# Optimization experiments

Hardware: AMD Instinct MI355X
Metric: run time of the kernel (lower is better)

Reference implementation:

```python
import jax, jax.numpy as jnp
import numpy as np

DMODEL = 1024
DK = 64
DHEAD = 16
DEPTH = DK * DHEAD
N, LQ, L = 4, 4096, 4096
FAC1 = 1.0 / np.sqrt(DK)  # relu kernel scale folded into omega, as in reset()
EPS = 1e-6


def setup_inputs() -> dict:
    key = jax.random.key(0)
    ks = jax.random.split(key, 10)
    x = jax.random.normal(ks[0], (N, LQ, DMODEL), jnp.float32)
    y = jax.random.normal(ks[1], (N, L, DMODEL), jnp.float32)
    s_in = 1.0 / np.sqrt(DMODEL)
    s_depth = 1.0 / np.sqrt(DEPTH)
    # Linear weights stored as (in, out) so application is x @ W + b
    WQ = jax.random.normal(ks[2], (DMODEL, DEPTH), jnp.float32) * s_in
    WK = jax.random.normal(ks[3], (DMODEL, DEPTH), jnp.float32) * s_in
    WV = jax.random.normal(ks[4], (DMODEL, DEPTH), jnp.float32) * s_in
    WO = jax.random.normal(ks[5], (DEPTH, DMODEL), jnp.float32) * s_depth
    bQ = jnp.zeros((DEPTH,), jnp.float32)
    bK = jnp.zeros((DEPTH,), jnp.float32)
    bV = jnp.zeros((DEPTH,), jnp.float32)
    bO = jnp.zeros((DMODEL,), jnp.float32)
    # orthogonal random-feature projection: QR of gaussian, scaled by sqrt(dk), then *fac1 (relu)
    g = np.random.default_rng(0).standard_normal((DK, DK)).astype(np.float32)
    qmat, _ = np.linalg.qr(g)
    omega = jnp.asarray(qmat * np.sqrt(DK) * FAC1, dtype=jnp.float32)
    return dict(x=x, y=y, WQ=WQ, bQ=bQ, WK=WK, bK=bK, WV=WV, bV=bV,
                WO=WO, bO=bO, omega=omega)


def reference(x, y, WQ, bQ, WK, bK, WV, bV, WO, bO, omega):
    n, lq, _ = x.shape
    l = y.shape[1]
    # project and split heads: (n, h, L, dk)
    q = (x @ WQ + bQ).reshape(n, lq, DHEAD, DK).transpose(0, 2, 1, 3)
    k = (y @ WK + bK).reshape(n, l, DHEAD, DK).transpose(0, 2, 1, 3)
    v = (y @ WV + bV).reshape(n, l, DHEAD, DK).transpose(0, 2, 1, 3)
    # relu random-feature map phi(x) = relu(x @ omega) + eps
    q = jax.nn.relu(q @ omega) + EPS
    k = jax.nn.relu(k @ omega) + EPS
    # linear attention: out = phi(q) @ (phi(k)^T @ v) / (phi(q) @ phi(k)^T @ 1)
    kv = jnp.einsum('nhld,nhle->nhde', k, v)          # (n, h, dk, dk)
    ksum = jnp.sum(k, axis=2)                          # (n, h, dk)
    d_inv = jnp.einsum('nhqd,nhd->nhq', q, ksum)[..., None]
    out = jnp.einsum('nhqd,nhde->nhqe', q, kv) / d_inv  # (n, h, Lq, dk)
    out = out.transpose(0, 2, 1, 3).reshape(n, lq, DEPTH)
    return out @ WO + bO
```

## Files before the change

kernel.cpp:

```cpp
#include <hip/hip_runtime.h>

#define EPSF 1e-6f

typedef _Float16 f16x8 __attribute__((ext_vector_type(8)));
typedef _Float16 f16x4 __attribute__((ext_vector_type(4)));
typedef float    f32x4 __attribute__((ext_vector_type(4)));

#define GLL16(gp, lp) __builtin_amdgcn_global_load_lds( \
    (const __attribute__((address_space(1))) void*)(gp), \
    (__attribute__((address_space(3))) void*)(lp), 16, 0, 0)

__global__ __launch_bounds__(256) void cvt_f16(const float* __restrict__ in,
                                               _Float16* __restrict__ out, int n8) {
    int idx = blockIdx.x * 256 + threadIdx.x;
    int stride = gridDim.x * 256;
    for (; idx < n8; idx += stride) {
        const float4* p = (const float4*)in + (size_t)idx * 2;
        float4 a = p[0], b = p[1];
        f16x8 o;
        o[0] = (_Float16)a.x; o[1] = (_Float16)a.y; o[2] = (_Float16)a.z; o[3] = (_Float16)a.w;
        o[4] = (_Float16)b.x; o[5] = (_Float16)b.y; o[6] = (_Float16)b.z; o[7] = (_Float16)b.w;
        *(f16x8*)(out + (size_t)idx * 8) = o;
    }
}

__global__ __launch_bounds__(256) void build_obdT(const float* __restrict__ omega,
                                                  _Float16* __restrict__ obdT) {
    int idx = blockIdx.x * 256 + threadIdx.x;
    int c = idx >> 10, k = idx & 1023;
    float v = ((c >> 6) == (k >> 6)) ? omega[(k & 63) * 64 + (c & 63)] : 0.f;
    obdT[idx] = (_Float16)v;
}

__global__ __launch_bounds__(256) void transpose_cvt(const float* __restrict__ in,
                                                     _Float16* __restrict__ out) {
    __shared__ float tile[64][65];
    const int t = threadIdx.x;
    const int k0 = blockIdx.x * 64, n0 = blockIdx.y * 64;
#pragma unroll
    for (int j = 0; j < 16; j++) {
        int idx = j * 256 + t; int r = idx >> 6, c = idx & 63;
        tile[r][c] = in[(size_t)(k0 + r) * 1024 + n0 + c];
    }
    __syncthreads();
#pragma unroll
    for (int j = 0; j < 16; j++) {
        int idx = j * 256 + t; int rn = idx >> 6, ck = idx & 63;
        out[(size_t)(n0 + rn) * 1024 + k0 + ck] = (_Float16)tile[ck][rn];
    }
}

__global__ __launch_bounds__(256) void fold_bias(const float* __restrict__ b,
                                                 const float* __restrict__ omega,
                                                 float* __restrict__ bout) {
    int c = blockIdx.x * 256 + threadIdx.x;
    int h = c >> 6, e = c & 63;
    float s = 0.f;
    for (int d = 0; d < 64; d++) s += b[h * 64 + d] * omega[d * 64 + e];
    bout[c] = s;
}

__global__ __launch_bounds__(256) void copy_f32(const float* __restrict__ in,
                                                float* __restrict__ out, int n) {
    int i = blockIdx.x * 256 + threadIdx.x;
    if (i < n) out[i] = in[i];
}

__global__ __launch_bounds__(256) void gemm_fold(const _Float16* __restrict__ A,
                                                 const _Float16* __restrict__ Bt,
                                                 _Float16* __restrict__ out0,
                                                 _Float16* __restrict__ out1) {
    const int K = 1024;
    __shared__ __align__(16) _Float16 Asm[128 * 32];
    __shared__ __align__(16) _Float16 Bsm[128 * 32];
    const int t = threadIdx.x, lane = t & 63, w = t >> 6;
    const int bm = blockIdx.y * 128, bn = blockIdx.x * 128;
    const int wm = (w >> 1) * 64, wn = (w & 1) * 64;
    const int r15 = lane & 15, slog = lane >> 4;

    int aoff[4], boff[4];
#pragma unroll
    for (int m = 0; m < 4; m++) {
        int ra = wm + m * 16 + r15;
        aoff[m] = ra * 32 + (slog ^ ((ra >> 1) & 3)) * 8;
        int rb = wn + m * 16 + r15;
        boff[m] = rb * 32 + (slog ^ ((rb >> 1) & 3)) * 8;
    }
    f32x4 acc[4][4];
#pragma unroll
    for (int m = 0; m < 4; m++)
#pragma unroll
        for (int n = 0; n < 4; n++) acc[m][n] = (f32x4){0.f, 0.f, 0.f, 0.f};

    for (int kt = 0; kt < K; kt += 32) {
        __syncthreads();
#pragma unroll
        for (int i = 0; i < 2; i++) {
            int seg = i * 256 + w * 64 + lane;
            int r = seg >> 2, sp = seg & 3;
            int sg = sp ^ ((r >> 1) & 3);
            GLL16(A  + (size_t)(bm + r) * K + kt + sg * 8, Asm + (size_t)(i * 256 + w * 64) * 8);
            GLL16(Bt + (size_t)(bn + r) * K + kt + sg * 8, Bsm + (size_t)(i * 256 + w * 64) * 8);
        }
        __syncthreads();
        f16x8 av[4], bv[4];
#pragma unroll
        for (int m = 0; m < 4; m++) av[m] = *(const f16x8*)(Asm + aoff[m]);
#pragma unroll
        for (int n = 0; n < 4; n++) bv[n] = *(const f16x8*)(Bsm + boff[n]);
#pragma unroll
        for (int m = 0; m < 4; m++)
#pragma unroll
            for (int n = 0; n < 4; n++)
                acc[m][n] = __builtin_amdgcn_mfma_f32_16x16x32_f16(av[m], bv[n], acc[m][n], 0, 0, 0);
    }

#pragma unroll
    for (int m = 0; m < 4; m++) {
        int row0 = bm + wm + m * 16 + slog * 4;
        _Float16* C = (row0 < 1024) ? out0 : out1;
        int l = row0 & 1023;
#pragma unroll
        for (int n = 0; n < 4; n++) {
            int colg = bn + wn + n * 16 + r15;
            f16x4 p;
#pragma unroll
            for (int j = 0; j < 4; j++) p[j] = (_Float16)acc[m][n][j];
            *(f16x4*)(C + (size_t)colg * 1024 + l) = p;
        }
    }
}

template<int EPI>
__global__ __launch_bounds__(512, 2) void gemm256(const _Float16* __restrict__ A,
                                                  const _Float16* __restrict__ Bt,
                                                  const float* __restrict__ bias,
                                                  void* __restrict__ out0,
                                                  void* __restrict__ out1,
                                                  int M, int N, int K, int nbn) {
    __shared__ __align__(16) char lds[131072];
    const int t = threadIdx.x, lane = t & 63, w = t >> 6;
    const int nwg = gridDim.x;
    const int f = (blockIdx.x & 7) * (nwg >> 3) + (blockIdx.x >> 3);
    const int bm = (f / nbn) * 256, bn = (f % nbn) * 256;
    const int wm = (w & 1) * 128, wn = (w >> 1) * 64;
    const int r15 = lane & 15, hi = lane >> 4;
    const int srow = lane >> 2, sp = lane & 3;

    int aoff[8], boff[4];
#pragma unroll
    for (int m = 0; m < 8; m++) {
        int r = wm + m * 16 + r15;
        aoff[m] = r * 64 + (((hi + (r >> 1)) & 3) << 4);
    }
#pragma unroll
    for (int n = 0; n < 4; n++) {
        int r = wn + n * 16 + r15;
        boff[n] = r * 64 + (((hi + (r >> 1)) & 3) << 4);
    }

    f32x4 acc[8][4];
#pragma unroll
    for (int m = 0; m < 8; m++)
#pragma unroll
        for (int n = 0; n < 4; n++) acc[m][n] = (f32x4){0.f, 0.f, 0.f, 0.f};

    auto stage = [&](int s) {
        char* base = lds + (s & 3) * 32768;
        int kt = s * 32;
#pragma unroll
        for (int p = 0; p < 2; p++) {
            int row = w * 32 + p * 16 + srow;
            int sg = (sp - ((row >> 1) & 3)) & 3;
            GLL16(A  + (size_t)(bm + row) * K + kt + sg * 8, base + w * 2048 + p * 1024);
            GLL16(Bt + (size_t)(bn + row) * K + kt + sg * 8, base + 16384 + w * 2048 + p * 1024);
        }
    };

    const int NS = K >> 5;
    stage(0); stage(1); stage(2);
    for (int s = 0; s < NS; ++s) {
        if (s + 2 < NS)      asm volatile("s_waitcnt vmcnt(8)" ::: "memory");
        else if (s + 1 < NS) asm volatile("s_waitcnt vmcnt(4)" ::: "memory");
        else                 asm volatile("s_waitcnt vmcnt(0)" ::: "memory");
        asm volatile("s_barrier" ::: "memory");
        if (s + 3 < NS) stage(s + 3);
        const char* La = lds + (s & 3) * 32768;
        const char* Lb = La + 16384;
        f16x8 bv[4];
#pragma unroll
        for (int n = 0; n < 4; n++) bv[n] = *(const f16x8*)(Lb + boff[n]);
        f16x8 av[8];
#pragma unroll
        for (int m = 0; m < 8; m++) av[m] = *(const f16x8*)(La + aoff[m]);
        __builtin_amdgcn_s_setprio(1);
#pragma unroll
        for (int m = 0; m < 8; m++)
#pragma unroll
            for (int n = 0; n < 4; n++)
                acc[m][n] = __builtin_amdgcn_mfma_f32_16x16x32_f16(av[m], bv[n], acc[m][n], 0, 0, 0);
        __builtin_amdgcn_s_setprio(0);
    }

    if (EPI == 3) {
        asm volatile("s_barrier" ::: "memory");
        char* LW = lds + w * 16384;
        const int colg0 = bn + wn;
        const bool isK = colg0 < 1024;
        _Float16* Cb = isK ? (_Float16*)out0 : (_Float16*)out1;
        const int hd = (isK ? colg0 : colg0 - 1024) >> 6;
        const int nb = bm >> 12;
        const int l0 = (bm & 4095) + wm;
#pragma unroll
        for (int m = 0; m < 8; m++)
#pragma unroll
            for (int n = 0; n < 4; n++) {
                int d = n * 16 + r15;
                float bs = bias[colg0 + d];
                f16x4 pk;
#pragma unroll
                for (int j = 0; j < 4; j++) {
                    float xv = acc[m][n][j] + bs;
                    if (isK) xv = fmaxf(xv, 0.f) + EPSF;
                    pk[j] = (_Float16)xv;
                }
                *(f16x4*)(LW + d * 256 + ((m * 32 + hi * 8) ^ ((d & 15) << 4))) = pk;
            }
        _Float16* basep = Cb + (size_t)(nb * 16 + hd) * 64 * 4096 + l0;
#pragma unroll
        for (int pass = 0; pass < 16; pass++) {
            int d = pass * 4 + hi;
            f16x8 v = *(const f16x8*)(LW + d * 256 + ((r15 * 16) ^ ((d & 15) << 4)));
            *(f16x8*)(basep + (size_t)d * 4096 + r15 * 8) = v;
        }
    } else {
#pragma unroll
        for (int m = 0; m < 8; m++) {
            int row0 = bm + wm + m * 16 + hi * 4;
#pragma unroll
            for (int n = 0; n < 4; n++) {
                int colg = bn + wn + n * 16 + r15;
                float bs = bias ? bias[colg] : 0.f;
#pragma unroll
                for (int j = 0; j < 4; j++) {
                    float xv = acc[m][n][j] + bs;
                    if (EPI == 1) {
                        xv = fmaxf(xv, 0.f) + EPSF;
                        ((_Float16*)out0)[(size_t)(row0 + j) * N + colg] = (_Float16)xv;
                    } else {
                        ((float*)out0)[(size_t)(row0 + j) * N + colg] = xv;
                    }
                }
            }
        }
    }
}

__global__ __launch_bounds__(256) void ksum_kernel(const _Float16* __restrict__ KphiT,
                                                   float* __restrict__ ksum) {
    const int t = threadIdx.x, lane = t & 63, w = t >> 6;
    const int gid = blockIdx.x;
    const int head = gid >> 4;
    const int d = (gid & 15) * 4 + w;
    const _Float16* src = KphiT + ((size_t)head * 64 + d) * 4096;
    float s = 0.f;
#pragma unroll
    for (int i = 0; i < 8; i++) {
        f16x8 v = *(const f16x8*)(src + (size_t)(i * 64 + lane) * 8);
#pragma unroll
        for (int j = 0; j < 8; j++) s += (float)v[j];
    }
#pragma unroll
    for (int o = 32; o; o >>= 1) s += __shfl_xor(s, o, 64);
    if (lane == 0) ksum[(size_t)head * 64 + d] = s;
}

__global__ __launch_bounds__(256) void kvt_kernel(const _Float16* __restrict__ Vt,
                                                  const _Float16* __restrict__ KphiT,
                                                  float* __restrict__ kvpart) {
    const int t = threadIdx.x, lane = t & 63, w = t >> 6;
    const int head = blockIdx.y;
    const int l0 = blockIdx.x * 1024;
    __shared__ __align__(16) _Float16 As[64 * 128];
    __shared__ __align__(16) _Float16 Bs[64 * 128];
    const int r15 = lane & 15, slog = lane >> 4;
    f32x4 acc[4][4];
#pragma unroll
    for (int m = 0; m < 4; m++)
#pragma unroll
        for (int n = 0; n < 4; n++) acc[m][n] = (f32x4){0.f, 0.f, 0.f, 0.f};

    for (int it = 0; it < 8; it++) {
        __syncthreads();
        int lbase = l0 + it * 128;
#pragma unroll
        for (int i = 0; i < 4; i++) {
            int seg = i * 256 + w * 64 + lane;
            int r = seg >> 4, sp2 = seg & 15;
            int sg = sp2 ^ (r & 15);
            GLL16(Vt    + ((size_t)head * 64 + r) * 4096 + lbase + sg * 8, As + (size_t)(i * 256 + w * 64) * 8);
            GLL16(KphiT + ((size_t)head * 64 + r) * 4096 + lbase + sg * 8, Bs + (size_t)(i * 256 + w * 64) * 8);
        }
        __syncthreads();
        f16x8 av[4], bv[4];
#pragma unroll
        for (int m = 0; m < 4; m++) {
            int r = m * 16 + r15;
            int s2 = w * 4 + slog;
            int ph = s2 ^ (r & 15);
            av[m] = *(const f16x8*)(As + r * 128 + ph * 8);
            bv[m] = *(const f16x8*)(Bs + r * 128 + ph * 8);
        }
#pragma unroll
        for (int m = 0; m < 4; m++)
#pragma unroll
            for (int n = 0; n < 4; n++)
                acc[m][n] = __builtin_amdgcn_mfma_f32_16x16x32_f16(av[m], bv[n], acc[m][n], 0, 0, 0);
    }
    float* red = (float*)As;
    for (int ww = 0; ww < 4; ww++) {
        __syncthreads();
        if (w == ww) {
#pragma unroll
            for (int m = 0; m < 4; m++)
#pragma unroll
                for (int n = 0; n < 4; n++)
#pragma unroll
                    for (int j = 0; j < 4; j++) {
                        int row = m * 16 + slog * 4 + j, col = n * 16 + r15;
                        if (ww == 0) red[row * 64 + col] = acc[m][n][j];
                        else         red[row * 64 + col] += acc[m][n][j];
                    }
        }
    }
    __syncthreads();
    float* outp = kvpart + ((size_t)head * 4 + blockIdx.x) * 4096;
#pragma unroll
    for (int i = 0; i < 16; i++) { int idx = i * 256 + t; outp[idx] = red[idx]; }
}

__global__ __launch_bounds__(256) void kvreduce(const float* __restrict__ kvpart,
                                                float* __restrict__ kvT) {
    int head = blockIdx.x, t = threadIdx.x;
#pragma unroll
    for (int i = 0; i < 16; i++) {
        int idx = i * 256 + t;
        float s = 0.f;
#pragma unroll
        for (int c = 0; c < 4; c++) s += kvpart[((size_t)head * 4 + c) * 4096 + idx];
        kvT[(size_t)head * 4096 + idx] = s;
    }
}

__global__ __launch_bounds__(256) void numdiv_kernel(const _Float16* __restrict__ Qphi,
                                                     const float* __restrict__ kvT,
                                                     const float* __restrict__ ksum,
                                                     _Float16* __restrict__ U) {
    const int t = threadIdx.x, lane = t & 63, w = t >> 6;
    const int h = blockIdx.y;
    const int m0 = blockIdx.x * 256;
    const int nb = m0 >> 12;
    const int head = nb * 16 + h;
    __shared__ __align__(16) _Float16 Qs[256 * 64];
    __shared__ __align__(16) _Float16 Bs[64 * 64];
    __shared__ float ksl[64];

#pragma unroll
    for (int i = 0; i < 8; i++) {
        int seg = i * 256 + w * 64 + lane;
        int r = seg >> 3, sp = seg & 7;
        int sg = sp ^ (r & 7);
        GLL16(Qphi + (size_t)(m0 + r) * 1024 + h * 64 + sg * 8, Qs + (size_t)(i * 256 + w * 64) * 8);
    }
#pragma unroll
    for (int i = 0; i < 2; i++) {
        int sidx = i * 256 + t;
        int r = sidx >> 3, p = sidx & 7;
        int sg = p ^ (r & 7);
        const float4* src = (const float4*)(kvT + (size_t)head * 4096 + r * 64 + sg * 8);
        float4 v0 = src[0], v1 = src[1];
        f16x8 o;
        o[0] = (_Float16)v0.x; o[1] = (_Float16)v0.y; o[2] = (_Float16)v0.z; o[3] = (_Float16)v0.w;
        o[4] = (_Float16)v1.x; o[5] = (_Float16)v1.y; o[6] = (_Float16)v1.z; o[7] = (_Float16)v1.w;
        *(f16x8*)(Bs + sidx * 8) = o;
    }
    if (t < 64) ksl[t] = ksum[(size_t)head * 64 + t];
    __syncthreads();

    const int r15 = lane & 15, slog = lane >> 4;
    f32x4 acc[4][4];
#pragma unroll
    for (int m = 0; m < 4; m++)
#pragma unroll
        for (int n = 0; n < 4; n++) acc[m][n] = (f32x4){0.f, 0.f, 0.f, 0.f};
    float dp[4] = {0.f, 0.f, 0.f, 0.f};

#pragma unroll
    for (int kk = 0; kk < 2; kk++) {
        float ks[8];
#pragma unroll
        for (int j = 0; j < 8; j++) ks[j] = ksl[kk * 32 + slog * 8 + j];
        f16x8 av[4], bv[4];
#pragma unroll
        for (int m = 0; m < 4; m++) {
            int r = w * 64 + m * 16 + r15;
            int ph = (kk * 4 + slog) ^ (r & 7);
            av[m] = *(const f16x8*)(Qs + r * 64 + ph * 8);
        }
#pragma unroll
        for (int n = 0; n < 4; n++) {
            int r = n * 16 + r15;
            int ph = (kk * 4 + slog) ^ (r & 7);
            bv[n] = *(const f16x8*)(Bs + r * 64 + ph * 8);
        }
#pragma unroll
        for (int m = 0; m < 4; m++)
#pragma unroll
            for (int j = 0; j < 8; j++) dp[m] += (float)av[m][j] * ks[j];
#pragma unroll
        for (int m = 0; m < 4; m++)
#pragma unroll
            for (int n = 0; n < 4; n++)
                acc[m][n] = __builtin_amdgcn_mfma_f32_16x16x32_f16(av[m], bv[n], acc[m][n], 0, 0, 0);
    }
#pragma unroll
    for (int m = 0; m < 4; m++) {
        dp[m] += __shfl_xor(dp[m], 16, 64);
        dp[m] += __shfl_xor(dp[m], 32, 64);
    }
#pragma unroll
    for (int m = 0; m < 4; m++) {
#pragma unroll
        for (int j = 0; j < 4; j++) {
            float den = __shfl(dp[m], slog * 4 + j, 64);
            float inv = __builtin_amdgcn_rcpf(den);
            int row = m0 + w * 64 + m * 16 + slog * 4 + j;
#pragma unroll
            for (int n = 0; n < 4; n++)
                U[(size_t)row * 1024 + h * 64 + n * 16 + r15] = (_Float16)(acc[m][n][j] * inv);
        }
    }
}

extern "C" void kernel_launch(void* const* d_in, const int* in_sizes, int n_in,
                              void* d_out, int out_size, void* d_ws, size_t ws_size,
                              hipStream_t stream) {
    (void)in_sizes; (void)n_in; (void)out_size; (void)ws_size;
    const float* x     = (const float*)d_in[0];
    const float* y     = (const float*)d_in[1];
    const float* WQ    = (const float*)d_in[2];
    const float* bQ    = (const float*)d_in[3];
    const float* WK    = (const float*)d_in[4];
    const float* bK    = (const float*)d_in[5];
    const float* WV    = (const float*)d_in[6];
    const float* bV    = (const float*)d_in[7];
    const float* WO    = (const float*)d_in[8];
    const float* bO    = (const float*)d_in[9];
    const float* omega = (const float*)d_in[10];

    char* ws = (char*)d_ws;
    size_t off = 0;
    auto alloc = [&](size_t bytes) { void* p = ws + off; off += (bytes + 255) & ~(size_t)255; return p; };
    const size_t BIG = (size_t)16384 * 1024 * 2;
    _Float16* xb    = (_Float16*)alloc(BIG);
    _Float16* yb    = (_Float16*)alloc(BIG);
    _Float16* WQKb  = (_Float16*)alloc((size_t)2048 * 1024 * 2);
    _Float16* obdT  = (_Float16*)alloc(1024 * 1024 * 2);
    _Float16* Wqt   = (_Float16*)alloc(1024 * 1024 * 2);
    _Float16* Wkvt  = (_Float16*)alloc((size_t)2048 * 1024 * 2);
    _Float16* Wot   = (_Float16*)alloc(1024 * 1024 * 2);
    float*    bQf   = (float*)alloc(1024 * 4);
    float*    bkv   = (float*)alloc(2048 * 4);
    _Float16* Qphi  = (_Float16*)alloc(BIG);
    _Float16* KphiT = (_Float16*)alloc(BIG);
    _Float16* Vt    = (_Float16*)alloc(BIG);
    float*    kvpart= (float*)alloc((size_t)256 * 4096 * 4);
    float*    kvT   = (float*)alloc((size_t)64 * 4096 * 4);
    float*    ksum  = (float*)alloc((size_t)64 * 64 * 4);
    _Float16* U     = xb;

    cvt_f16<<<2048, 256, 0, stream>>>(x, xb, 16384 * 1024 / 8);
    cvt_f16<<<2048, 256, 0, stream>>>(y, yb, 16384 * 1024 / 8);
    cvt_f16<<<512, 256, 0, stream>>>(WQ, WQKb, 1024 * 1024 / 8);
    cvt_f16<<<512, 256, 0, stream>>>(WK, WQKb + (size_t)1024 * 1024, 1024 * 1024 / 8);
    build_obdT<<<4096, 256, 0, stream>>>(omega, obdT);
    transpose_cvt<<<dim3(16, 16), 256, 0, stream>>>(WV, Wkvt + (size_t)1024 * 1024);
    transpose_cvt<<<dim3(16, 16), 256, 0, stream>>>(WO, Wot);
    fold_bias<<<4, 256, 0, stream>>>(bQ, omega, bQf);
    fold_bias<<<4, 256, 0, stream>>>(bK, omega, bkv);
    copy_f32<<<4, 256, 0, stream>>>(bV, bkv + 1024, 1024);
    gemm_fold<<<dim3(8, 16), 256, 0, stream>>>(WQKb, obdT, Wqt, Wkvt);
    gemm256<1><<<256, 512, 0, stream>>>(xb, Wqt, bQf, Qphi, nullptr, 16384, 1024, 1024, 4);
    gemm256<3><<<512, 512, 0, stream>>>(yb, Wkvt, bkv, KphiT, Vt, 16384, 2048, 1024, 8);
    ksum_kernel<<<1024, 256, 0, stream>>>(KphiT, ksum);
    kvt_kernel<<<dim3(4, 64), 256, 0, stream>>>(Vt, KphiT, kvpart);
    kvreduce<<<64, 256, 0, stream>>>(kvpart, kvT);
    numdiv_kernel<<<dim3(64, 16), 256, 0, stream>>>(Qphi, kvT, ksum, U);
    gemm256<2><<<256, 512, 0, stream>>>(U, Wot, bO, d_out, nullptr, 16384, 1024, 1024, 4);
}
```

Before: 287.2 us.

## Split GEMM main loop into interleaved halves and fuse small prep/reduce kernels

The gemm256 main loop now issues the next stage's async loads first, then splits the MFMA work into two halves (low and high A rows). Extra barriers and waitcnts let LDS reads for the second half overlap with compute on the first. Separately, the three bias-prep kernels are merged into one, and the kvreduce kernel is removed by summing the four kv partials directly inside numdiv. This cuts launch count and one intermediate buffer round trip, in exchange for more barriers per GEMM iteration and redundant partial reads across numdiv blocks.

Measured after the change: 288.0 us. No clear change (+0.3%).

```diff
diff --git a/kernel.cpp b/kernel.cpp
--- a/kernel.cpp
+++ b/kernel.cpp
@@ -50,20 +50,23 @@
     }
 }
 
-__global__ __launch_bounds__(256) void fold_bias(const float* __restrict__ b,
+__global__ __launch_bounds__(256) void prep_bias(const float* __restrict__ bQ,
+                                                 const float* __restrict__ bK,
+                                                 const float* __restrict__ bV,
                                                  const float* __restrict__ omega,
-                                                 float* __restrict__ bout) {
+                                                 float* __restrict__ bQf,
+                                                 float* __restrict__ bkv) {
     int c = blockIdx.x * 256 + threadIdx.x;
     int h = c >> 6, e = c & 63;
-    float s = 0.f;
-    for (int d = 0; d < 64; d++) s += b[h * 64 + d] * omega[d * 64 + e];
-    bout[c] = s;
-}
-
-__global__ __launch_bounds__(256) void copy_f32(const float* __restrict__ in,
-                                                float* __restrict__ out, int n) {
-    int i = blockIdx.x * 256 + threadIdx.x;
-    if (i < n) out[i] = in[i];
+    float sq = 0.f, sk = 0.f;
+    for (int d = 0; d < 64; d++) {
+        float o = omega[d * 64 + e];
+        sq += bQ[h * 64 + d] * o;
+        sk += bK[h * 64 + d] * o;
+    }
+    bQf[c] = sq;
+    bkv[c] = sk;
+    bkv[1024 + c] = bV[c];
 }
 
 __global__ __launch_bounds__(256) void gemm_fold(const _Float16* __restrict__ A,
@@ -179,31 +182,46 @@
 
     const int NS = K >> 5;
     stage(0); stage(1); stage(2);
+    asm volatile("s_waitcnt vmcnt(8)" ::: "memory");
+    asm volatile("s_barrier" ::: "memory");
     for (int s = 0; s < NS; ++s) {
-        if (s + 2 < NS)      asm volatile("s_waitcnt vmcnt(8)" ::: "memory");
-        else if (s + 1 < NS) asm volatile("s_waitcnt vmcnt(4)" ::: "memory");
+        const char* La = lds + (s & 3) * 32768;
+        const char* Lb = La + 16384;
+        if (s + 3 < NS) stage(s + 3);
+        f16x8 bv[4], avL[4];
+#pragma unroll
+        for (int n = 0; n < 4; n++) bv[n] = *(const f16x8*)(Lb + boff[n]);
+#pragma unroll
+        for (int m = 0; m < 4; m++) avL[m] = *(const f16x8*)(La + aoff[m]);
+        asm volatile("s_barrier" ::: "memory");
+        asm volatile("s_waitcnt lgkmcnt(0)" ::: "memory");
+        __builtin_amdgcn_s_setprio(1);
+#pragma unroll
+        for (int m = 0; m < 4; m++)
+#pragma unroll
+            for (int n = 0; n < 4; n++)
+                acc[m][n] = __builtin_amdgcn_mfma_f32_16x16x32_f16(avL[m], bv[n], acc[m][n], 0, 0, 0);
+        __builtin_amdgcn_s_setprio(0);
+        asm volatile("s_barrier" ::: "memory");
+        f16x8 avH[4];
+#pragma unroll
+        for (int m = 0; m < 4; m++) avH[m] = *(const f16x8*)(La + aoff[m + 4]);
+        if (s + 3 < NS)      asm volatile("s_waitcnt vmcnt(8)" ::: "memory");
+        else if (s + 2 < NS) asm volatile("s_waitcnt vmcnt(4)" ::: "memory");
         else                 asm volatile("s_waitcnt vmcnt(0)" ::: "memory");
         asm volatile("s_barrier" ::: "memory");
-        if (s + 3 < NS) stage(s + 3);
-        const char* La = lds + (s & 3) * 32768;
-        const char* Lb = La + 16384;
-        f16x8 bv[4];
-#pragma unroll
-        for (int n = 0; n < 4; n++) bv[n] = *(const f16x8*)(Lb + boff[n]);
-        f16x8 av[8];
-#pragma unroll
-        for (int m = 0; m < 8; m++) av[m] = *(const f16x8*)(La + aoff[m]);
+        asm volatile("s_waitcnt lgkmcnt(0)" ::: "memory");
         __builtin_amdgcn_s_setprio(1);
 #pragma unroll
-        for (int m = 0; m < 8; m++)
+        for (int m = 0; m < 4; m++)
 #pragma unroll
             for (int n = 0; n < 4; n++)
-                acc[m][n] = __builtin_amdgcn_mfma_f32_16x16x32_f16(av[m], bv[n], acc[m][n], 0, 0, 0);
+                acc[m + 4][n] = __builtin_amdgcn_mfma_f32_16x16x32_f16(avH[m], bv[n], acc[m + 4][n], 0, 0, 0);
         __builtin_amdgcn_s_setprio(0);
+        asm volatile("s_barrier" ::: "memory");
     }
 
     if (EPI == 3) {
-        asm volatile("s_barrier" ::: "memory");
         char* LW = lds + w * 16384;
         const int colg0 = bn + wn;
         const bool isK = colg0 < 1024;
@@ -339,21 +357,8 @@
     for (int i = 0; i < 16; i++) { int idx = i * 256 + t; outp[idx] = red[idx]; }
 }
 
-__global__ __launch_bounds__(256) void kvreduce(const float* __restrict__ kvpart,
-                                                float* __restrict__ kvT) {
-    int head = blockIdx.x, t = threadIdx.x;
-#pragma unroll
-    for (int i = 0; i < 16; i++) {
-        int idx = i * 256 + t;
-        float s = 0.f;
-#pragma unroll
-        for (int c = 0; c < 4; c++) s += kvpart[((size_t)head * 4 + c) * 4096 + idx];
-        kvT[(size_t)head * 4096 + idx] = s;
-    }
-}
-
 __global__ __launch_bounds__(256) void numdiv_kernel(const _Float16* __restrict__ Qphi,
-                                                     const float* __restrict__ kvT,
+                                                     const float* __restrict__ kvpart,
                                                      const float* __restrict__ ksum,
                                                      _Float16* __restrict__ U) {
     const int t = threadIdx.x, lane = t & 63, w = t >> 6;
@@ -377,8 +382,15 @@
         int sidx = i * 256 + t;
         int r = sidx >> 3, p = sidx & 7;
         int sg = p ^ (r & 7);
-        const float4* src = (const float4*)(kvT + (size_t)head * 4096 + r * 64 + sg * 8);
-        float4 v0 = src[0], v1 = src[1];
+        const float* s0 = kvpart + (size_t)head * 4 * 4096 + r * 64 + sg * 8;
+        float4 v0 = {0.f, 0.f, 0.f, 0.f}, v1 = {0.f, 0.f, 0.f, 0.f};
+#pragma unroll
+        for (int c = 0; c < 4; c++) {
+            float4 a = *(const float4*)(s0 + c * 4096);
+            float4 b = *(const float4*)(s0 + c * 4096 + 4);
+            v0.x += a.x; v0.y += a.y; v0.z += a.z; v0.w += a.w;
+            v1.x += b.x; v1.y += b.y; v1.z += b.z; v1.w += b.w;
+        }
         f16x8 o;
         o[0] = (_Float16)v0.x; o[1] = (_Float16)v0.y; o[2] = (_Float16)v0.z; o[3] = (_Float16)v0.w;
         o[4] = (_Float16)v1.x; o[5] = (_Float16)v1.y; o[6] = (_Float16)v1.z; o[7] = (_Float16)v1.w;
@@ -475,7 +487,6 @@
     _Float16* KphiT = (_Float16*)alloc(BIG);
     _Float16* Vt    = (_Float16*)alloc(BIG);
     float*    kvpart= (float*)alloc((size_t)256 * 4096 * 4);
-    float*    kvT   = (float*)alloc((size_t)64 * 4096 * 4);
     float*    ksum  = (float*)alloc((size_t)64 * 64 * 4);
     _Float16* U     = xb;
 
@@ -486,15 +497,12 @@
     build_obdT<<<4096, 256, 0, stream>>>(omega, obdT);
     transpose_cvt<<<dim3(16, 16), 256, 0, stream>>>(WV, Wkvt + (size_t)1024 * 1024);
     transpose_cvt<<<dim3(16, 16), 256, 0, stream>>>(WO, Wot);
-    fold_bias<<<4, 256, 0, stream>>>(bQ, omega, bQf);
-    fold_bias<<<4, 256, 0, stream>>>(bK, omega, bkv);
-    copy_f32<<<4, 256, 0, stream>>>(bV, bkv + 1024, 1024);
+    prep_bias<<<4, 256, 0, stream>>>(bQ, bK, bV, omega, bQf, bkv);
     gemm_fold<<<dim3(8, 16), 256, 0, stream>>>(WQKb, obdT, Wqt, Wkvt);
     gemm256<1><<<256, 512, 0, stream>>>(xb, Wqt, bQf, Qphi, nullptr, 16384, 1024, 1024, 4);
     gemm256<3><<<512, 512, 0, stream>>>(yb, Wkvt, bkv, KphiT, Vt, 16384, 2048, 1024, 8);
     ksum_kernel<<<1024, 256, 0, stream>>>(KphiT, ksum);
     kvt_kernel<<<dim3(4, 64), 256, 0, stream>>>(Vt, KphiT, kvpart);
-    kvreduce<<<64, 256, 0, stream>>>(kvpart, kvT);
-    numdiv_kernel<<<dim3(64, 16), 256, 0, stream>>>(Qphi, kvT, ksum, U);
+    numdiv_kernel<<<dim3(64, 16), 256, 0, stream>>>(Qphi, kvpart, ksum, U);
     gemm256<2><<<256, 512, 0, stream>>>(U, Wot, bO, d_out, nullptr, 16384, 1024, 1024, 4);
 }
```

## Fold kv state into per-batch output weights and fuse normalization into Q GEMM

Applied to the files above, without the earlier changes.

Reassociates the attention output so each batch's kv matrix is premultiplied into WO, producing a per-batch W2 used by the final GEMM. This removes the numdiv kernel and kvreduce pass. The Q-projection GEMM now applies phi and the per-row denominator division in its epilogue, and the K/V GEMM epilogue accumulates ksum with atomics, so the separate ksum kernel is gone. Small prep kernels are merged into fewer launches. The cost is a new w2t kernel plus extra rounding from fp16 W2 with a 1/4096 scale, and atomic-order nondeterminism in ksum.

After: 280.2 us. 2.5% less time.

```diff
diff --git a/kernel.cpp b/kernel.cpp
--- a/kernel.cpp
+++ b/kernel.cpp
@@ -10,26 +10,46 @@
     (const __attribute__((address_space(1))) void*)(gp), \
     (__attribute__((address_space(3))) void*)(lp), 16, 0, 0)
 
-__global__ __launch_bounds__(256) void cvt_f16(const float* __restrict__ in,
-                                               _Float16* __restrict__ out, int n8) {
+__global__ __launch_bounds__(256) void cvt2_f16(const float* __restrict__ inA,
+                                                _Float16* __restrict__ outA,
+                                                const float* __restrict__ inB,
+                                                _Float16* __restrict__ outB, int n8each) {
     int idx = blockIdx.x * 256 + threadIdx.x;
-    int stride = gridDim.x * 256;
-    for (; idx < n8; idx += stride) {
-        const float4* p = (const float4*)in + (size_t)idx * 2;
-        float4 a = p[0], b = p[1];
-        f16x8 o;
-        o[0] = (_Float16)a.x; o[1] = (_Float16)a.y; o[2] = (_Float16)a.z; o[3] = (_Float16)a.w;
-        o[4] = (_Float16)b.x; o[5] = (_Float16)b.y; o[6] = (_Float16)b.z; o[7] = (_Float16)b.w;
-        *(f16x8*)(out + (size_t)idx * 8) = o;
-    }
-}
-
-__global__ __launch_bounds__(256) void build_obdT(const float* __restrict__ omega,
-                                                  _Float16* __restrict__ obdT) {
+    const float* in = inA; _Float16* out = outA;
+    if (idx >= n8each) { idx -= n8each; in = inB; out = outB; }
+    const float4* p = (const float4*)in + (size_t)idx * 2;
+    float4 a = p[0], b = p[1];
+    f16x8 o;
+    o[0] = (_Float16)a.x; o[1] = (_Float16)a.y; o[2] = (_Float16)a.z; o[3] = (_Float16)a.w;
+    o[4] = (_Float16)b.x; o[5] = (_Float16)b.y; o[6] = (_Float16)b.z; o[7] = (_Float16)b.w;
+    *(f16x8*)(out + (size_t)idx * 8) = o;
+}
+
+__global__ __launch_bounds__(256) void prep_all(const float* __restrict__ omega,
+                                                const float* __restrict__ bQ,
+                                                const float* __restrict__ bK,
+                                                const float* __restrict__ bV,
+                                                _Float16* __restrict__ obdT,
+                                                float* __restrict__ bQf,
+                                                float* __restrict__ bkv,
+                                                float* __restrict__ ksum) {
     int idx = blockIdx.x * 256 + threadIdx.x;
     int c = idx >> 10, k = idx & 1023;
     float v = ((c >> 6) == (k >> 6)) ? omega[(k & 63) * 64 + (c & 63)] : 0.f;
     obdT[idx] = (_Float16)v;
+    if (idx < 4096) ksum[idx] = 0.f;
+    if (idx < 1024) {
+        int h = idx >> 6, e = idx & 63;
+        float sq = 0.f, sk = 0.f;
+        for (int d = 0; d < 64; d++) {
+            float o = omega[d * 64 + e];
+            sq += bQ[h * 64 + d] * o;
+            sk += bK[h * 64 + d] * o;
+        }
+        bQf[idx] = sq;
+        bkv[idx] = sk;
+        bkv[1024 + idx] = bV[idx];
+    }
 }
 
 __global__ __launch_bounds__(256) void transpose_cvt(const float* __restrict__ in,
@@ -48,22 +68,6 @@
         int idx = j * 256 + t; int rn = idx >> 6, ck = idx & 63;
         out[(size_t)(n0 + rn) * 1024 + k0 + ck] = (_Float16)tile[ck][rn];
     }
-}
-
-__global__ __launch_bounds__(256) void fold_bias(const float* __restrict__ b,
-                                                 const float* __restrict__ omega,
-                                                 float* __restrict__ bout) {
-    int c = blockIdx.x * 256 + threadIdx.x;
-    int h = c >> 6, e = c & 63;
-    float s = 0.f;
-    for (int d = 0; d < 64; d++) s += b[h * 64 + d] * omega[d * 64 + e];
-    bout[c] = s;
-}
-
-__global__ __launch_bounds__(256) void copy_f32(const float* __restrict__ in,
-                                                float* __restrict__ out, int n) {
-    int i = blockIdx.x * 256 + threadIdx.x;
-    if (i < n) out[i] = in[i];
 }
 
 __global__ __launch_bounds__(256) void gemm_fold(const _Float16* __restrict__ A,
@@ -137,6 +141,7 @@
                                                   const float* __restrict__ bias,
                                                   void* __restrict__ out0,
                                                   void* __restrict__ out1,
+                                                  float* __restrict__ ksum,
                                                   int M, int N, int K, int nbn) {
     __shared__ __align__(16) char lds[131072];
     const int t = threadIdx.x, lane = t & 63, w = t >> 6;
@@ -146,6 +151,7 @@
     const int wm = (w & 1) * 128, wn = (w >> 1) * 64;
     const int r15 = lane & 15, hi = lane >> 4;
     const int srow = lane >> 2, sp = lane & 3;
+    const _Float16* BtU = (EPI == 2) ? Bt + ((size_t)(bm >> 12) << 20) : Bt;
 
     int aoff[8], boff[4];
 #pragma unroll
@@ -172,8 +178,8 @@
         for (int p = 0; p < 2; p++) {
             int row = w * 32 + p * 16 + srow;
             int sg = (sp - ((row >> 1) & 3)) & 3;
-            GLL16(A  + (size_t)(bm + row) * K + kt + sg * 8, base + w * 2048 + p * 1024);
-            GLL16(Bt + (size_t)(bn + row) * K + kt + sg * 8, base + 16384 + w * 2048 + p * 1024);
+            GLL16(A   + (size_t)(bm + row) * K + kt + sg * 8, base + w * 2048 + p * 1024);
+            GLL16(BtU + (size_t)(bn + row) * K + kt + sg * 8, base + 16384 + w * 2048 + p * 1024);
         }
     };
 
@@ -211,6 +217,7 @@
         const int hd = (isK ? colg0 : colg0 - 1024) >> 6;
         const int nb = bm >> 12;
         const int l0 = (bm & 4095) + wm;
+        float cs[4] = {0.f, 0.f, 0.f, 0.f};
 #pragma unroll
         for (int m = 0; m < 8; m++)
 #pragma unroll
@@ -221,11 +228,23 @@
 #pragma unroll
                 for (int j = 0; j < 4; j++) {
                     float xv = acc[m][n][j] + bs;
-                    if (isK) xv = fmaxf(xv, 0.f) + EPSF;
+                    if (isK) { xv = fmaxf(xv, 0.f) + EPSF; cs[n] += xv; }
                     pk[j] = (_Float16)xv;
                 }
                 *(f16x4*)(LW + d * 256 + ((m * 32 + hi * 8) ^ ((d & 15) << 4))) = pk;
             }
+        if (isK) {
+#pragma unroll
+            for (int n = 0; n < 4; n++) {
+                cs[n] += __shfl_xor(cs[n], 16, 64);
+                cs[n] += __shfl_xor(cs[n], 32, 64);
+            }
+            if (hi == 0) {
+#pragma unroll
+                for (int n = 0; n < 4; n++)
+                    atomicAdd(ksum + (size_t)(nb * 16 + hd) * 64 + n * 16 + r15, cs[n]);
+            }
+        }
         _Float16* basep = Cb + (size_t)(nb * 16 + hd) * 64 * 4096 + l0;
 #pragma unroll
         for (int pass = 0; pass < 16; pass++) {
@@ -233,6 +252,44 @@
             f16x8 v = *(const f16x8*)(LW + d * 256 + ((r15 * 16) ^ ((d & 15) << 4)));
             *(f16x8*)(basep + (size_t)d * 4096 + r15 * 8) = v;
         }
+    } else if (EPI == 4) {
+        const int headg = (bm >> 12) * 16 + ((bn + wn) >> 6);
+        const float* ks = (const float*)out1;
+        float ksn[4];
+#pragma unroll
+        for (int n = 0; n < 4; n++) ksn[n] = ks[(size_t)headg * 64 + n * 16 + r15];
+        _Float16* C = (_Float16*)out0;
+#pragma unroll
+        for (int m = 0; m < 8; m++) {
+            int row0 = bm + wm + m * 16 + hi * 4;
+            float qv[4][4], dp[4] = {0.f, 0.f, 0.f, 0.f};
+#pragma unroll
+            for (int n = 0; n < 4; n++) {
+                int colg = bn + wn + n * 16 + r15;
+                float bs = bias[colg];
+#pragma unroll
+                for (int j = 0; j < 4; j++) {
+                    float xv = fmaxf(acc[m][n][j] + bs, 0.f) + EPSF;
+                    qv[n][j] = xv;
+                    dp[j] += xv * ksn[n];
+                }
+            }
+#pragma unroll
+            for (int j = 0; j < 4; j++) {
+                dp[j] += __shfl_xor(dp[j], 1, 64);
+                dp[j] += __shfl_xor(dp[j], 2, 64);
+                dp[j] += __shfl_xor(dp[j], 4, 64);
+                dp[j] += __shfl_xor(dp[j], 8, 64);
+                dp[j] = 4096.0f * __builtin_amdgcn_rcpf(dp[j]);
+            }
+#pragma unroll
+            for (int n = 0; n < 4; n++) {
+                int colg = bn + wn + n * 16 + r15;
+#pragma unroll
+                for (int j = 0; j < 4; j++)
+                    C[(size_t)(row0 + j) * N + colg] = (_Float16)(qv[n][j] * dp[j]);
+            }
+        }
     } else {
 #pragma unroll
         for (int m = 0; m < 8; m++) {
@@ -242,37 +299,11 @@
                 int colg = bn + wn + n * 16 + r15;
                 float bs = bias ? bias[colg] : 0.f;
 #pragma unroll
-                for (int j = 0; j < 4; j++) {
-                    float xv = acc[m][n][j] + bs;
-                    if (EPI == 1) {
-                        xv = fmaxf(xv, 0.f) + EPSF;
-                        ((_Float16*)out0)[(size_t)(row0 + j) * N + colg] = (_Float16)xv;
-                    } else {
-                        ((float*)out0)[(size_t)(row0 + j) * N + colg] = xv;
-                    }
-                }
-            }
-        }
-    }
-}
-
-__global__ __launch_bounds__(256) void ksum_kernel(const _Float16* __restrict__ KphiT,
-                                                   float* __restrict__ ksum) {
-    const int t = threadIdx.x, lane = t & 63, w = t >> 6;
-    const int gid = blockIdx.x;
-    const int head = gid >> 4;
-    const int d = (gid & 15) * 4 + w;
-    const _Float16* src = KphiT + ((size_t)head * 64 + d) * 4096;
-    float s = 0.f;
-#pragma unroll
-    for (int i = 0; i < 8; i++) {
-        f16x8 v = *(const f16x8*)(src + (size_t)(i * 64 + lane) * 8);
-#pragma unroll
-        for (int j = 0; j < 8; j++) s += (float)v[j];
-    }
-#pragma unroll
-    for (int o = 32; o; o >>= 1) s += __shfl_xor(s, o, 64);
-    if (lane == 0) ksum[(size_t)head * 64 + d] = s;
+                for (int j = 0; j < 4; j++)
+                    ((float*)out0)[(size_t)(row0 + j) * N + colg] = acc[m][n][j] + bs;
+            }
+        }
+    }
 }
 
 __global__ __launch_bounds__(256) void kvt_kernel(const _Float16* __restrict__ Vt,
@@ -339,106 +370,41 @@
     for (int i = 0; i < 16; i++) { int idx = i * 256 + t; outp[idx] = red[idx]; }
 }
 
-__global__ __launch_bounds__(256) void kvreduce(const float* __restrict__ kvpart,
-                                                float* __restrict__ kvT) {
-    int head = blockIdx.x, t = threadIdx.x;
+__global__ __launch_bounds__(256) void w2t_kernel(const _Float16* __restrict__ Wot,
+                                                  const float* __restrict__ kvpart,
+                                                  _Float16* __restrict__ W2t) {
+    const int t = threadIdx.x;
+    const int jb = blockIdx.x;
+    const int gh = blockIdx.y;
+    const int b = gh >> 4, hl = gh & 15;
+    __shared__ float kvL[64][65];
+    const float* kp = kvpart + (size_t)gh * 4 * 4096;
 #pragma unroll
     for (int i = 0; i < 16; i++) {
         int idx = i * 256 + t;
         float s = 0.f;
 #pragma unroll
-        for (int c = 0; c < 4; c++) s += kvpart[((size_t)head * 4 + c) * 4096 + idx];
-        kvT[(size_t)head * 4096 + idx] = s;
-    }
-}
-
-__global__ __launch_bounds__(256) void numdiv_kernel(const _Float16* __restrict__ Qphi,
-                                                     const float* __restrict__ kvT,
-                                                     const float* __restrict__ ksum,
-                                                     _Float16* __restrict__ U) {
-    const int t = threadIdx.x, lane = t & 63, w = t >> 6;
-    const int h = blockIdx.y;
-    const int m0 = blockIdx.x * 256;
-    const int nb = m0 >> 12;
-    const int head = nb * 16 + h;
-    __shared__ __align__(16) _Float16 Qs[256 * 64];
-    __shared__ __align__(16) _Float16 Bs[64 * 64];
-    __shared__ float ksl[64];
-
+        for (int c = 0; c < 4; c++) s += kp[c * 4096 + idx];
+        kvL[idx >> 6][idx & 63] = s;
+    }
+    __syncthreads();
+    const int j = jb * 128 + (t >> 1);
+    const int d0 = (t & 1) * 32;
+    const _Float16* wr = Wot + (size_t)j * 1024 + hl * 64;
+    float wv[64];
 #pragma unroll
     for (int i = 0; i < 8; i++) {
-        int seg = i * 256 + w * 64 + lane;
-        int r = seg >> 3, sp = seg & 7;
-        int sg = sp ^ (r & 7);
-        GLL16(Qphi + (size_t)(m0 + r) * 1024 + h * 64 + sg * 8, Qs + (size_t)(i * 256 + w * 64) * 8);
-    }
-#pragma unroll
-    for (int i = 0; i < 2; i++) {
-        int sidx = i * 256 + t;
-        int r = sidx >> 3, p = sidx & 7;
-        int sg = p ^ (r & 7);
-        const float4* src = (const float4*)(kvT + (size_t)head * 4096 + r * 64 + sg * 8);
-        float4 v0 = src[0], v1 = src[1];
-        f16x8 o;
-        o[0] = (_Float16)v0.x; o[1] = (_Float16)v0.y; o[2] = (_Float16)v0.z; o[3] = (_Float16)v0.w;
-        o[4] = (_Float16)v1.x; o[5] = (_Float16)v1.y; o[6] = (_Float16)v1.z; o[7] = (_Float16)v1.w;
-        *(f16x8*)(Bs + sidx * 8) = o;
-    }
-    if (t < 64) ksl[t] = ksum[(size_t)head * 64 + t];
-    __syncthreads();
-
-    const int r15 = lane & 15, slog = lane >> 4;
-    f32x4 acc[4][4];
-#pragma unroll
-    for (int m = 0; m < 4; m++)
-#pragma unroll
-        for (int n = 0; n < 4; n++) acc[m][n] = (f32x4){0.f, 0.f, 0.f, 0.f};
-    float dp[4] = {0.f, 0.f, 0.f, 0.f};
-
-#pragma unroll
-    for (int kk = 0; kk < 2; kk++) {
-        float ks[8];
-#pragma unroll
-        for (int j = 0; j < 8; j++) ks[j] = ksl[kk * 32 + slog * 8 + j];
-        f16x8 av[4], bv[4];
-#pragma unroll
-        for (int m = 0; m < 4; m++) {
-            int r = w * 64 + m * 16 + r15;
-            int ph = (kk * 4 + slog) ^ (r & 7);
-            av[m] = *(const f16x8*)(Qs + r * 64 + ph * 8);
-        }
-#pragma unroll
-        for (int n = 0; n < 4; n++) {
-            int r = n * 16 + r15;
-            int ph = (kk * 4 + slog) ^ (r & 7);
-            bv[n] = *(const f16x8*)(Bs + r * 64 + ph * 8);
-        }
-#pragma unroll
-        for (int m = 0; m < 4; m++)
-#pragma unroll
-            for (int j = 0; j < 8; j++) dp[m] += (float)av[m][j] * ks[j];
-#pragma unroll
-        for (int m = 0; m < 4; m++)
-#pragma unroll
-            for (int n = 0; n < 4; n++)
-                acc[m][n] = __builtin_amdgcn_mfma_f32_16x16x32_f16(av[m], bv[n], acc[m][n], 0, 0, 0);
-    }
-#pragma unroll
-    for (int m = 0; m < 4; m++) {
-        dp[m] += __shfl_xor(dp[m], 16, 64);
-        dp[m] += __shfl_xor(dp[m], 32, 64);
-    }
-#pragma unroll
-    for (int m = 0; m < 4; m++) {
-#pragma unroll
-        for (int j = 0; j < 4; j++) {
-            float den = __shfl(dp[m], slog * 4 + j, 64);
-            float inv = __builtin_amdgcn_rcpf(den);
-            int row = m0 + w * 64 + m * 16 + slog * 4 + j;
-#pragma unroll
-            for (int n = 0; n < 4; n++)
-                U[(size_t)row * 1024 + h * 64 + n * 16 + r15] = (_Float16)(acc[m][n][j] * inv);
-        }
+        f16x8 v = *(const f16x8*)(wr + i * 8);
+#pragma unroll
+        for (int k = 0; k < 8; k++) wv[i * 8 + k] = (float)v[k];
+    }
+    _Float16* outp = W2t + ((size_t)b << 20) + (size_t)j * 1024 + hl * 64 + d0;
+#pragma unroll
+    for (int d = 0; d < 32; d++) {
+        float s = 0.f;
+#pragma unroll
+        for (int e = 0; e < 64; e++) s += wv[e] * kvL[e][d0 + d];
+        outp[d] = (_Float16)(s * (1.0f / 4096.0f));
     }
 }
 
@@ -469,32 +435,24 @@
     _Float16* Wqt   = (_Float16*)alloc(1024 * 1024 * 2);
     _Float16* Wkvt  = (_Float16*)alloc((size_t)2048 * 1024 * 2);
     _Float16* Wot   = (_Float16*)alloc(1024 * 1024 * 2);
+    _Float16* W2t   = (_Float16*)alloc((size_t)4 * 1024 * 1024 * 2);
     float*    bQf   = (float*)alloc(1024 * 4);
     float*    bkv   = (float*)alloc(2048 * 4);
-    _Float16* Qphi  = (_Float16*)alloc(BIG);
+    _Float16* U2    = (_Float16*)alloc(BIG);
     _Float16* KphiT = (_Float16*)alloc(BIG);
     _Float16* Vt    = (_Float16*)alloc(BIG);
     float*    kvpart= (float*)alloc((size_t)256 * 4096 * 4);
-    float*    kvT   = (float*)alloc((size_t)64 * 4096 * 4);
     float*    ksum  = (float*)alloc((size_t)64 * 64 * 4);
-    _Float16* U     = xb;
-
-    cvt_f16<<<2048, 256, 0, stream>>>(x, xb, 16384 * 1024 / 8);
-    cvt_f16<<<2048, 256, 0, stream>>>(y, yb, 16384 * 1024 / 8);
-    cvt_f16<<<512, 256, 0, stream>>>(WQ, WQKb, 1024 * 1024 / 8);
-    cvt_f16<<<512, 256, 0, stream>>>(WK, WQKb + (size_t)1024 * 1024, 1024 * 1024 / 8);
-    build_obdT<<<4096, 256, 0, stream>>>(omega, obdT);
+
+    cvt2_f16<<<16384, 256, 0, stream>>>(x, xb, y, yb, 16384 * 1024 / 8);
+    cvt2_f16<<<1024, 256, 0, stream>>>(WQ, WQKb, WK, WQKb + (size_t)1024 * 1024, 1024 * 1024 / 8);
+    prep_all<<<4096, 256, 0, stream>>>(omega, bQ, bK, bV, obdT, bQf, bkv, ksum);
     transpose_cvt<<<dim3(16, 16), 256, 0, stream>>>(WV, Wkvt + (size_t)1024 * 1024);
     transpose_cvt<<<dim3(16, 16), 256, 0, stream>>>(WO, Wot);
-    fold_bias<<<4, 256, 0, stream>>>(bQ, omega, bQf);
-    fold_bias<<<4, 256, 0, stream>>>(bK, omega, bkv);
-    copy_f32<<<4, 256, 0, stream>>>(bV, bkv + 1024, 1024);
     gemm_fold<<<dim3(8, 16), 256, 0, stream>>>(WQKb, obdT, Wqt, Wkvt);
-    gemm256<1><<<256, 512, 0, stream>>>(xb, Wqt, bQf, Qphi, nullptr, 16384, 1024, 1024, 4);
-    gemm256<3><<<512, 512, 0, stream>>>(yb, Wkvt, bkv, KphiT, Vt, 16384, 2048, 1024, 8);
-    ksum_kernel<<<1024, 256, 0, stream>>>(KphiT, ksum);
+    gemm256<3><<<512, 512, 0, stream>>>(yb, Wkvt, bkv, KphiT, Vt, ksum, 16384, 2048, 1024, 8);
     kvt_kernel<<<dim3(4, 64), 256, 0, stream>>>(Vt, KphiT, kvpart);
-    kvreduce<<<64, 256, 0, stream>>>(kvpart, kvT);
-    numdiv_kernel<<<dim3(64, 16), 256, 0, stream>>>(Qphi, kvT, ksum, U);
-    gemm256<2><<<256, 512, 0, stream>>>(U, Wot, bO, d_out, nullptr, 16384, 1024, 1024, 4);
-}
+    w2t_kernel<<<dim3(8, 64), 256, 0, stream>>>(Wot, kvpart, W2t);
+    gemm256<4><<<256, 512, 0, stream>>>(xb, Wqt, bQf, U2, ksum, nullptr, 16384, 1024, 1024, 4);
+    gemm256<2><<<256, 512, 0, stream>>>(U2, W2t, bO, d_out, nullptr, nullptr, 16384, 1024, 1024, 4);
+}
```
